# Optimization experiments

Hardware: AMD Instinct MI355X
Metric: run time of the kernel (lower is better)

Reference implementation:

```python
import jax, jax.numpy as jnp
import numpy as np

B, L, E, H, Dff = 2, 2048, 1024, 16, 4096
Dh = E // H


def _ln(x, g, b, eps=1e-5):
    m = jnp.mean(x, axis=-1, keepdims=True)
    v = jnp.mean((x - m) ** 2, axis=-1, keepdims=True)
    return (x - m) / jnp.sqrt(v + eps) * g + b


def setup_inputs() -> dict:
    key = jax.random.key(0)
    ks = jax.random.split(key, 16)
    s_e = 1.0 / np.sqrt(E)
    s_d = 1.0 / np.sqrt(Dff)
    inp = {
        "x": jax.random.normal(ks[0], (B, L, E), jnp.float32),
        # causal mask: positions with 0 are masked out (masked_fill(mask==0, -1e9))
        "mask": jnp.tril(jnp.ones((L, L), jnp.bool_)),
        # per-head QKV projections, stacked over heads: (H, E, Dh), biases (H, Dh)
        "Wq": jax.random.uniform(ks[1], (H, E, Dh), jnp.float32, -s_e, s_e),
        "bq": jax.random.uniform(ks[2], (H, Dh), jnp.float32, -s_e, s_e),
        "Wk": jax.random.uniform(ks[3], (H, E, Dh), jnp.float32, -s_e, s_e),
        "bk": jax.random.uniform(ks[4], (H, Dh), jnp.float32, -s_e, s_e),
        "Wv": jax.random.uniform(ks[5], (H, E, Dh), jnp.float32, -s_e, s_e),
        "bv": jax.random.uniform(ks[6], (H, Dh), jnp.float32, -s_e, s_e),
        "Wo": jax.random.uniform(ks[7], (E, E), jnp.float32, -s_e, s_e),
        "bo": jax.random.uniform(ks[8], (E,), jnp.float32, -s_e, s_e),
        "W1": jax.random.uniform(ks[9], (E, Dff), jnp.float32, -s_e, s_e),
        "c1": jax.random.uniform(ks[10], (Dff,), jnp.float32, -s_e, s_e),
        "W2": jax.random.uniform(ks[11], (Dff, E), jnp.float32, -s_d, s_d),
        "c2": jax.random.uniform(ks[12], (E,), jnp.float32, -s_d, s_d),
        "g1": jnp.ones((E,), jnp.float32),
        "beta1": jnp.zeros((E,), jnp.float32),
        "g2": jnp.ones((E,), jnp.float32),
        "beta2": jnp.zeros((E,), jnp.float32),
    }
    return inp


def reference(x, mask, Wq, bq, Wk, bk, Wv, bv, Wo, bo, W1, c1, W2, c2, g1, beta1, g2, beta2):
    # Batched equivalent of the per-head Attention loop (eval mode: dropout = identity)
    q = jnp.einsum("ble,hed->bhld", x, Wq) + bq[None, :, None, :]
    k = jnp.einsum("ble,hed->bhld", x, Wk) + bk[None, :, None, :]
    v = jnp.einsum("ble,hed->bhld", x, Wv) + bv[None, :, None, :]
    scores = jnp.einsum("bhld,bhmd->bhlm", q, k) / np.sqrt(Dh).astype(np.float32)
    scores = jnp.where(mask[None, None, :, :], scores, -1e9)
    p = jax.nn.softmax(scores, axis=-1)
    z = jnp.einsum("bhlm,bhmd->bhld", p, v)  # (B,H,L,Dh)
    z = z.transpose(0, 2, 1, 3).reshape(B, L, E)  # concat heads
    att = z @ Wo + bo
    h = _ln(x + att, g1, beta1)
    ff = jax.nn.relu(h @ W1 + c1) @ W2 + c2
    out = _ln(h + ff, g2, beta2)
    return out
```

## Files before the change

### kernel.cpp

```cpp
#include <hip/hip_runtime.h>
#include <hip/hip_bf16.h>
#include <math.h>

#define B_   2
#define L_   2048
#define E_   1024
#define H_   16
#define DH   64
#define DFF  4096
#define M_   4096
#define APAD 72
#define SCALE_Q 0.18033688011112042f

typedef __attribute__((ext_vector_type(8))) short short8;
typedef __attribute__((ext_vector_type(4))) float f32x4;
typedef __bf16 bf16x8 __attribute__((ext_vector_type(8)));

__device__ __forceinline__ float bf2f(unsigned short u) {
    return __uint_as_float(((unsigned)u) << 16);
}
__device__ __forceinline__ unsigned short f2bf(float f) {
    unsigned u = __float_as_uint(f);
    return (unsigned short)((u + 0x7fff + ((u >> 16) & 1)) >> 16);
}
__device__ __forceinline__ unsigned pk_trunc(float lo, float hi) {
    return (__float_as_uint(lo) >> 16) | (__float_as_uint(hi) & 0xffff0000u);
}

__device__ __forceinline__ void gld16(const unsigned short* g, unsigned short* l) {
    __builtin_amdgcn_global_load_lds(
        (const __attribute__((address_space(1))) void*)g,
        (__attribute__((address_space(3))) void*)l, 16, 0, 0);
}

__global__ __launch_bounds__(256) void prep(const float* __restrict__ x,
                                            const float* __restrict__ Wq,
                                            const float* __restrict__ Wk,
                                            const float* __restrict__ Wv,
                                            const float* __restrict__ bq,
                                            const float* __restrict__ bk,
                                            const float* __restrict__ bv,
                                            const float* __restrict__ Wo,
                                            const float* __restrict__ W1,
                                            const float* __restrict__ W2,
                                            unsigned short* __restrict__ xb,
                                            unsigned short* __restrict__ Wqkvt,
                                            unsigned short* __restrict__ Wot,
                                            unsigned short* __restrict__ W1t,
                                            unsigned short* __restrict__ W2t,
                                            float* __restrict__ bqkv) {
    __shared__ float tile[32][33];
    int bid = blockIdx.x;
    const int t = threadIdx.x;

    if (bid < 4096) {
        int i = (bid * 256 + t) * 4;
        float4 v = *(const float4*)&x[i];
        ushort4 pk = { f2bf(v.x), f2bf(v.y), f2bf(v.z), f2bf(v.w) };
        *(ushort4*)&xb[i] = pk;
        return;
    }
    bid -= 4096;

    const float* in; unsigned short* outp; int R, C, r0, c0; float sc = 1.f;
    if (bid < 3072) {
        int xq = bid & 1, yq = (bid >> 1) & 31, wh = bid >> 6;
        int which = wh >> 4, h = wh & 15;
        in   = (which == 0 ? Wq : which == 1 ? Wk : Wv) + (size_t)h * E_ * DH;
        outp = Wqkvt + ((size_t)which * 1024 + h * 64) * 1024;
        R = E_; C = DH; r0 = yq * 32; c0 = xq * 32;
        if (which == 0) sc = SCALE_Q;
    } else if (bid < 4096) {
        bid -= 3072;
        in = Wo; outp = Wot; R = E_; C = E_;
        c0 = (bid & 31) * 32; r0 = (bid >> 5) * 32;
    } else if (bid < 8192) {
        bid -= 4096;
        in = W1; outp = W1t; R = E_; C = DFF;
        c0 = (bid & 127) * 32; r0 = (bid >> 7) * 32;
    } else if (bid < 12288) {
        bid -= 8192;
        in = W2; outp = W2t; R = DFF; C = E_;
        c0 = (bid & 31) * 32; r0 = (bid >> 5) * 32;
    } else {
        bid -= 12288;
        int n = bid * 256 + t;
        bqkv[n] = n < 1024 ? bq[n] * SCALE_Q : n < 2048 ? bk[n - 1024] : bv[n - 2048];
        return;
    }

    const int tx = t & 31, tq = t >> 5;
#pragma unroll
    for (int s2 = 0; s2 < 4; s2++)
        tile[tq * 4 + s2][tx] = in[(size_t)(r0 + tq * 4 + s2) * C + c0 + tx] * sc;
    __syncthreads();
#pragma unroll
    for (int s2 = 0; s2 < 4; s2++)
        outp[(size_t)(c0 + tq * 4 + s2) * R + r0 + tx] = f2bf(tile[tx][tq * 4 + s2]);
}

__global__ __launch_bounds__(256) void v_transpose_perm(const unsigned short* __restrict__ qkv,
                                                        unsigned short* __restrict__ vtg) {
    __shared__ unsigned short tile[64 * APAD];
    const int t  = threadIdx.x;
    const int kt = blockIdx.x, hh = blockIdx.y, b = blockIdx.z;
    const int rr0 = t >> 3, o8 = (t & 7) * 8, rr1 = rr0 + 32;
    const size_t gbase = ((size_t)b * L_ + kt * 64) * 3072 + 2048 + hh * 64;
    *(short8*)&tile[rr0 * APAD + o8] = *(const short8*)&qkv[gbase + (size_t)rr0 * 3072 + o8];
    *(short8*)&tile[rr1 * APAD + o8] = *(const short8*)&qkv[gbase + (size_t)rr1 * 3072 + o8];
    __syncthreads();
    const size_t obase = ((size_t)(b * H_ + hh) * 64) * (size_t)L_ + kt * 64;
    const int a = t & 15, d0 = (t >> 4) * 4;
#pragma unroll
    for (int s2 = 0; s2 < 4; s2++) {
        int d = d0 + s2;
        ushort4 pk = { tile[(a +  0) * APAD + d], tile[(a + 16) * APAD + d],
                       tile[(a + 32) * APAD + d], tile[(a + 48) * APAD + d] };
        *(ushort4*)&vtg[obase + (size_t)d * L_ + 4 * a] = pk;
    }
}

template <int RELU, int OUT_BF16>
__global__ __launch_bounds__(256) void gemm_bt(const unsigned short* __restrict__ A,
                                               const unsigned short* __restrict__ Bt,
                                               const float* __restrict__ bias,
                                               void* __restrict__ Cout,
                                               int M, int N, int K) {
    __shared__ __align__(16) unsigned short As[2][128 * 32];
    __shared__ __align__(16) unsigned short Bs[2][128 * 32];

    const int t    = threadIdx.x;
    const int lane = t & 63;
    const int w    = t >> 6;
    const int quad = lane >> 4;
    const int l16  = lane & 15;
    const int wm = (w >> 1) * 64, wn = (w & 1) * 64;

    const int lin = blockIdx.x;
    const int xcd = lin & 7, s = lin >> 3;
    const int n0 = (s >> 2) * 128;
    const int m0 = ((xcd << 2) | (s & 3)) * 128;
    const int rowA = t >> 2, offA = (t & 3) * 8, rowA2 = rowA + 64;

    const size_t aoff0 = (size_t)(m0 + rowA)  * K + offA;
    const size_t aoff1 = (size_t)(m0 + rowA2) * K + offA;
    const size_t boff0 = (size_t)(n0 + rowA)  * K + offA;
    const size_t boff1 = (size_t)(n0 + rowA2) * K + offA;

    const int wb0 = w * 512, wb1 = 2048 + w * 512;

    f32x4 acc[4][4];
#pragma unroll
    for (int i = 0; i < 4; i++)
#pragma unroll
        for (int j = 0; j < 4; j++) acc[i][j] = (f32x4){0.f, 0.f, 0.f, 0.f};

    gld16(&A[aoff0],  &As[0][wb0]);
    gld16(&A[aoff1],  &As[0][wb1]);
    gld16(&Bt[boff0], &Bs[0][wb0]);
    gld16(&Bt[boff1], &Bs[0][wb1]);
    __syncthreads();

    int p = 0;
    for (int k0 = 0; k0 < K; k0 += 32, p ^= 1) {
        if (k0 + 32 < K) {
            gld16(&A[aoff0 + k0 + 32],  &As[p ^ 1][wb0]);
            gld16(&A[aoff1 + k0 + 32],  &As[p ^ 1][wb1]);
            gld16(&Bt[boff0 + k0 + 32], &Bs[p ^ 1][wb0]);
            gld16(&Bt[boff1 + k0 + 32], &Bs[p ^ 1][wb1]);
        }

        bf16x8 af[4], bfv[4];
#pragma unroll
        for (int i = 0; i < 4; i++)
            af[i] = *(const bf16x8*)&As[p][(wm + i * 16 + l16) * 32 + quad * 8];
#pragma unroll
        for (int j = 0; j < 4; j++)
            bfv[j] = *(const bf16x8*)&Bs[p][(wn + j * 16 + l16) * 32 + quad * 8];
#pragma unroll
        for (int i = 0; i < 4; i++)
#pragma unroll
            for (int j = 0; j < 4; j++)
                acc[i][j] = __builtin_amdgcn_mfma_f32_16x16x32_bf16(af[i], bfv[j], acc[i][j], 0, 0, 0);

        __syncthreads();
    }

#pragma unroll
    for (int j = 0; j < 4; j++) {
        int col = n0 + wn + j * 16 + l16;
        float bv = bias[col];
#pragma unroll
        for (int i = 0; i < 4; i++) {
            int rowb = m0 + wm + i * 16 + quad * 4;
#pragma unroll
            for (int r = 0; r < 4; r++) {
                float v = acc[i][j][r] + bv;
                if (RELU) v = fmaxf(v, 0.f);
                if (OUT_BF16)
                    ((unsigned short*)Cout)[(size_t)(rowb + r) * N + col] = f2bf(v);
                else
                    ((float*)Cout)[(size_t)(rowb + r) * N + col] = v;
            }
        }
    }
}

__global__ __launch_bounds__(256) void gemm_sk4(const unsigned short* __restrict__ A,
                                                const unsigned short* __restrict__ Bt,
                                                unsigned short* __restrict__ P0,
                                                unsigned short* __restrict__ P1,
                                                unsigned short* __restrict__ P2,
                                                unsigned short* __restrict__ P3,
                                                int M, int N, int K, int Nt) {
    __shared__ __align__(16) unsigned short As[2][128 * 32];
    __shared__ __align__(16) unsigned short Bs[2][128 * 32];

    const int t    = threadIdx.x;
    const int lane = t & 63;
    const int w    = t >> 6;
    const int quad = lane >> 4;
    const int l16  = lane & 15;
    const int wm = (w >> 1) * 64, wn = (w & 1) * 64;

    const int lin = blockIdx.x;
    const int xcd = lin & 7, s = lin >> 3;
    const int mi = s & 3;
    const int r  = s >> 2;
    const int n0 = (r % Nt) * 128;
    const int z  = r / Nt;
    const int m0 = ((xcd << 2) | mi) * 128;

    const int K4 = K >> 2;
    const int kbeg = z * K4;
    unsigned short* C = (z == 0) ? P0 : (z == 1) ? P1 : (z == 2) ? P2 : P3;
    const int rowA = t >> 2, offA = (t & 3) * 8, rowA2 = rowA + 64;

    const size_t aoff0 = (size_t)(m0 + rowA)  * K + offA + kbeg;
    const size_t aoff1 = (size_t)(m0 + rowA2) * K + offA + kbeg;
    const size_t boff0 = (size_t)(n0 + rowA)  * K + offA + kbeg;
    const size_t boff1 = (size_t)(n0 + rowA2) * K + offA + kbeg;

    const int wb0 = w * 512, wb1 = 2048 + w * 512;

    f32x4 acc[4][4];
#pragma unroll
    for (int i = 0; i < 4; i++)
#pragma unroll
        for (int j = 0; j < 4; j++) acc[i][j] = (f32x4){0.f, 0.f, 0.f, 0.f};

    gld16(&A[aoff0],  &As[0][wb0]);
    gld16(&A[aoff1],  &As[0][wb1]);
    gld16(&Bt[boff0], &Bs[0][wb0]);
    gld16(&Bt[boff1], &Bs[0][wb1]);
    __syncthreads();

    int p = 0;
    for (int k0 = 0; k0 < K4; k0 += 32, p ^= 1) {
        if (k0 + 32 < K4) {
            gld16(&A[aoff0 + k0 + 32],  &As[p ^ 1][wb0]);
            gld16(&A[aoff1 + k0 + 32],  &As[p ^ 1][wb1]);
            gld16(&Bt[boff0 + k0 + 32], &Bs[p ^ 1][wb0]);
            gld16(&Bt[boff1 + k0 + 32], &Bs[p ^ 1][wb1]);
        }

        bf16x8 af[4], bfv[4];
#pragma unroll
        for (int i = 0; i < 4; i++)
            af[i] = *(const bf16x8*)&As[p][(wm + i * 16 + l16) * 32 + quad * 8];
#pragma unroll
        for (int j = 0; j < 4; j++)
            bfv[j] = *(const bf16x8*)&Bs[p][(wn + j * 16 + l16) * 32 + quad * 8];
#pragma unroll
        for (int i = 0; i < 4; i++)
#pragma unroll
            for (int j = 0; j < 4; j++)
                acc[i][j] = __builtin_amdgcn_mfma_f32_16x16x32_bf16(af[i], bfv[j], acc[i][j], 0, 0, 0);

        __syncthreads();
    }

#pragma unroll
    for (int j = 0; j < 4; j++) {
        int col = n0 + wn + j * 16 + l16;
#pragma unroll
        for (int i = 0; i < 4; i++) {
            int rowb = m0 + wm + i * 16 + quad * 4;
#pragma unroll
            for (int r2 = 0; r2 < 4; r2++)
                C[(size_t)(rowb + r2) * N + col] = f2bf(acc[i][j][r2]);
        }
    }
}

__global__ __launch_bounds__(256, 3) void attn_mfma(const unsigned short* __restrict__ qkv,
                                                    const unsigned short* __restrict__ vtg,
                                                    unsigned short* __restrict__ zb) {
    __shared__ __align__(16) unsigned short ks[2][64 * APAD];
    __shared__ __align__(16) unsigned short vt[64 * APAD];
    __shared__ __align__(16) unsigned short ps[128 * APAD];

    const int t    = threadIdx.x;
    const int lane = t & 63;
    const int w    = t >> 6;
    const int l16  = lane & 15;
    const int quad = lane >> 4;

    const int lin  = blockIdx.x;
    const int xcd  = lin & 7;
    const int s    = lin >> 3;
    const int hh   = xcd * 2 + (s & 1);
    const int rest = s >> 1;
    const int b    = rest & 1;
    const int qq0  = rest >> 1;
    const int qq   = b ? qq0 : 15 - qq0;

    const size_t rowbase = (size_t)b * L_;
    const size_t vbase   = ((size_t)(b * H_ + hh) * 64) * (size_t)L_;

    bf16x8 qf[2][2];
#pragma unroll
    for (int g = 0; g < 2; g++) {
        size_t qrow = rowbase + qq * 128 + w * 32 + g * 16 + l16;
#pragma unroll
        for (int c = 0; c < 2; c++)
            qf[g][c] = *(const bf16x8*)&qkv[qrow * 3072 + hh * 64 + c * 32 + quad * 8];
    }

    f32x4 o[2][4];
#pragma unroll
    for (int g = 0; g < 2; g++)
#pragma unroll
        for (int j = 0; j < 4; j++) o[g][j] = (f32x4){0.f, 0.f, 0.f, 0.f};
    float l_i[2][4] = {};

    const int rr0 = t >> 3, o8 = (t & 7) * 8, rr1 = rr0 + 32;
    const int ktmax = 2 * qq + 1;

    {
        size_t kg = rowbase * 3072 + 1024 + hh * 64;
        short8 k0 = *(const short8*)&qkv[kg + (size_t)rr0 * 3072 + o8];
        short8 k1 = *(const short8*)&qkv[kg + (size_t)rr1 * 3072 + o8];
        short8 v0 = *(const short8*)&vtg[vbase + (size_t)rr0 * L_ + o8];
        short8 v1 = *(const short8*)&vtg[vbase + (size_t)rr1 * L_ + o8];
        *(short8*)&ks[0][rr0 * APAD + o8] = k0;
        *(short8*)&ks[0][rr1 * APAD + o8] = k1;
        *(short8*)&vt[rr0 * APAD + o8] = v0;
        *(short8*)&vt[rr1 * APAD + o8] = v1;
    }

    short8 kr0, kr1, vr0, vr1;
    for (int kt = 0; kt <= ktmax; kt++) {
        const int p = kt & 1;
        __syncthreads();

        if (kt < ktmax) {
            size_t kg = (rowbase + (kt + 1) * 64) * 3072 + 1024 + hh * 64;
            kr0 = *(const short8*)&qkv[kg + (size_t)rr0 * 3072 + o8];
            kr1 = *(const short8*)&qkv[kg + (size_t)rr1 * 3072 + o8];
            size_t vg = vbase + (kt + 1) * 64;
            vr0 = *(const short8*)&vtg[vg + (size_t)rr0 * L_ + o8];
            vr1 = *(const short8*)&vtg[vg + (size_t)rr1 * L_ + o8];
        }

        f32x4 s4[2][4];
#pragma unroll
        for (int g = 0; g < 2; g++)
#pragma unroll
            for (int j = 0; j < 4; j++) s4[g][j] = (f32x4){0.f, 0.f, 0.f, 0.f};
#pragma unroll
        for (int c = 0; c < 2; c++)
#pragma unroll
            for (int j = 0; j < 4; j++) {
                bf16x8 kf = *(const bf16x8*)&ks[p][(j * 16 + l16) * APAD + c * 32 + quad * 8];
#pragma unroll
                for (int g = 0; g < 2; g++)
                    s4[g][j] = __builtin_amdgcn_mfma_f32_16x16x32_bf16(qf[g][c], kf, s4[g][j], 0, 0, 0);
            }

        if (kt >= 2 * qq) {
#pragma unroll
            for (int g = 0; g < 2; g++)
#pragma unroll
                for (int j = 0; j < 4; j++) {
                    int lk = kt * 64 + j * 16 + l16;
#pragma unroll
                    for (int r = 0; r < 4; r++)
                        if (lk > qq * 128 + w * 32 + g * 16 + quad * 4 + r)
                            s4[g][j][r] = -INFINITY;
                }
        }

#pragma unroll
        for (int g = 0; g < 2; g++)
#pragma unroll
            for (int r = 0; r < 4; r++) {
                float p0 = __builtin_amdgcn_exp2f(s4[g][0][r]);
                float p1 = __builtin_amdgcn_exp2f(s4[g][1][r]);
                float p2 = __builtin_amdgcn_exp2f(s4[g][2][r]);
                float p3 = __builtin_amdgcn_exp2f(s4[g][3][r]);
                l_i[g][r] += (p0 + p1) + (p2 + p3);
                uint2 pk = { pk_trunc(p0, p1), pk_trunc(p2, p3) };
                *(uint2*)&ps[(w * 32 + g * 16 + quad * 4 + r) * APAD + 4 * l16] = pk;
            }

        __builtin_amdgcn_s_waitcnt(0xc07f);

#pragma unroll
        for (int c = 0; c < 2; c++) {
            bf16x8 pf[2];
#pragma unroll
            for (int g = 0; g < 2; g++)
                pf[g] = *(const bf16x8*)&ps[(w * 32 + g * 16 + l16) * APAD + c * 32 + quad * 8];
#pragma unroll
            for (int j = 0; j < 4; j++) {
                bf16x8 vf = *(const bf16x8*)&vt[(j * 16 + l16) * APAD + c * 32 + quad * 8];
#pragma unroll
                for (int g = 0; g < 2; g++)
                    o[g][j] = __builtin_amdgcn_mfma_f32_16x16x32_bf16(pf[g], vf, o[g][j], 0, 0, 0);
            }
        }

        __syncthreads();
        if (kt < ktmax) {
            *(short8*)&ks[p ^ 1][rr0 * APAD + o8] = kr0;
            *(short8*)&ks[p ^ 1][rr1 * APAD + o8] = kr1;
            *(short8*)&vt[rr0 * APAD + o8] = vr0;
            *(short8*)&vt[rr1 * APAD + o8] = vr1;
        }
    }

#pragma unroll
    for (int g = 0; g < 2; g++)
#pragma unroll
        for (int r = 0; r < 4; r++) {
            float l = l_i[g][r];
            l += __shfl_xor(l, 1);
            l += __shfl_xor(l, 2);
            l += __shfl_xor(l, 4);
            l += __shfl_xor(l, 8);
            float inv = 1.f / l;
            size_t row = rowbase + qq * 128 + w * 32 + g * 16 + quad * 4 + r;
#pragma unroll
            for (int j = 0; j < 4; j++)
                zb[row * 1024 + hh * 64 + j * 16 + l16] = f2bf(o[g][j][r] * inv);
        }
}

template <int WRITE_BF16>
__global__ __launch_bounds__(256) void ln5_kernel(const float* __restrict__ a,
                                                  const unsigned short* __restrict__ q0,
                                                  const unsigned short* __restrict__ q1,
                                                  const unsigned short* __restrict__ q2,
                                                  const unsigned short* __restrict__ q3,
                                                  const float* __restrict__ bias,
                                                  const float* __restrict__ g,
                                                  const float* __restrict__ be,
                                                  float* __restrict__ out,
                                                  unsigned short* __restrict__ out_bf) {
    __shared__ float s1[256], s2[256];
    const int row = blockIdx.x;
    const int t   = threadIdx.x;
    const size_t base = (size_t)row * E_ + t * 4;

    float4 ya = *(const float4*)&a[base];
    ushort4 u0 = *(const ushort4*)&q0[base];
    ushort4 u1 = *(const ushort4*)&q1[base];
    ushort4 u2 = *(const ushort4*)&q2[base];
    ushort4 u3 = *(const ushort4*)&q3[base];
    float4 bb = *(const float4*)&bias[t * 4];
    float y0 = ya.x + bb.x + bf2f(u0.x) + bf2f(u1.x) + bf2f(u2.x) + bf2f(u3.x);
    float y1 = ya.y + bb.y + bf2f(u0.y) + bf2f(u1.y) + bf2f(u2.y) + bf2f(u3.y);
    float y2 = ya.z + bb.z + bf2f(u0.z) + bf2f(u1.z) + bf2f(u2.z) + bf2f(u3.z);
    float y3 = ya.w + bb.w + bf2f(u0.w) + bf2f(u1.w) + bf2f(u2.w) + bf2f(u3.w);

    s1[t] = y0 + y1 + y2 + y3;
    s2[t] = y0 * y0 + y1 * y1 + y2 * y2 + y3 * y3;
    __syncthreads();
    for (int off = 128; off > 0; off >>= 1) {
        if (t < off) { s1[t] += s1[t + off]; s2[t] += s2[t + off]; }
        __syncthreads();
    }
    float mean = s1[0] * (1.0f / E_);
    float var  = s2[0] * (1.0f / E_) - mean * mean;
    float rstd = rsqrtf(var + 1e-5f);

    float4 gv = *(const float4*)&g[t * 4];
    float4 bv = *(const float4*)&be[t * 4];
    float4 ov;
    ov.x = (y0 - mean) * rstd * gv.x + bv.x;
    ov.y = (y1 - mean) * rstd * gv.y + bv.y;
    ov.z = (y2 - mean) * rstd * gv.z + bv.z;
    ov.w = (y3 - mean) * rstd * gv.w + bv.w;
    *(float4*)&out[base] = ov;
    if (WRITE_BF16) {
        ushort4 pk = { f2bf(ov.x), f2bf(ov.y), f2bf(ov.z), f2bf(ov.w) };
        *(ushort4*)&out_bf[base] = pk;
    }
}

extern "C" void kernel_launch(void* const* d_in, const int* in_sizes, int n_in,
                              void* d_out, int out_size, void* d_ws, size_t ws_size,
                              hipStream_t stream)
{
    const float* x     = (const float*)d_in[0];
    const float* Wq    = (const float*)d_in[2];
    const float* bq    = (const float*)d_in[3];
    const float* Wk    = (const float*)d_in[4];
    const float* bk    = (const float*)d_in[5];
    const float* Wv    = (const float*)d_in[6];
    const float* bv    = (const float*)d_in[7];
    const float* Wo    = (const float*)d_in[8];
    const float* bo    = (const float*)d_in[9];
    const float* W1    = (const float*)d_in[10];
    const float* c1    = (const float*)d_in[11];
    const float* W2    = (const float*)d_in[12];
    const float* c2    = (const float*)d_in[13];
    const float* g1    = (const float*)d_in[14];
    const float* beta1 = (const float*)d_in[15];
    const float* g2    = (const float*)d_in[16];
    const float* beta2 = (const float*)d_in[17];
    float* out = (float*)d_out;

    const size_t MB = 1024 * 1024;
    char* w = (char*)d_ws;
    unsigned short* xb    = (unsigned short*)(w + 0 * MB);
    unsigned short* Wqkvt = (unsigned short*)(w + 8 * MB);
    unsigned short* Wot   = (unsigned short*)(w + 14 * MB);
    unsigned short* W1t   = (unsigned short*)(w + 16 * MB);
    unsigned short* W2t   = (unsigned short*)(w + 24 * MB);
    float*          bqkv  = (float*)(w + 32 * MB);
    unsigned short* qkv   = (unsigned short*)(w + 33 * MB);
    unsigned short* zb    = (unsigned short*)(w + 57 * MB);
    float*          h     = (float*)(w + 65 * MB);
    unsigned short* vtg   = (unsigned short*)(w + 89 * MB);
    unsigned short* ap0   = (unsigned short*)(w + 33 * MB);
    unsigned short* ap1   = (unsigned short*)(w + 41 * MB);
    unsigned short* ap2   = (unsigned short*)(w + 49 * MB);
    unsigned short* ap3   = (unsigned short*)(w + 89 * MB);
    unsigned short* hb    = (unsigned short*)(w + 0 * MB);
    unsigned short* ff1b  = (unsigned short*)(w + 33 * MB);
    unsigned short* fp0   = (unsigned short*)(w + 0 * MB);
    unsigned short* fp1   = (unsigned short*)(w + 8 * MB);
    unsigned short* fp2   = (unsigned short*)(w + 16 * MB);
    unsigned short* fp3   = (unsigned short*)(w + 81 * MB);

    dim3 blk(256);

    prep<<<dim3(16396), blk, 0, stream>>>(x, Wq, Wk, Wv, bq, bk, bv, Wo, W1, W2,
                                          xb, Wqkvt, Wot, W1t, W2t, bqkv);

    gemm_bt<0, 1><<<dim3(768), blk, 0, stream>>>(xb, Wqkvt, bqkv, qkv, M_, 3072, E_);

    v_transpose_perm<<<dim3(L_ / 64, H_, B_), blk, 0, stream>>>(qkv, vtg);

    attn_mfma<<<dim3(512), blk, 0, stream>>>(qkv, vtg, zb);

    gemm_sk4<<<dim3(1024), blk, 0, stream>>>(zb, Wot, ap0, ap1, ap2, ap3, M_, E_, E_, 8);

    ln5_kernel<1><<<dim3(M_), blk, 0, stream>>>(x, ap0, ap1, ap2, ap3, bo, g1, beta1, h, hb);

    gemm_bt<1, 1><<<dim3(1024), blk, 0, stream>>>(hb, W1t, c1, ff1b, M_, DFF, E_);

    gemm_sk4<<<dim3(1024), blk, 0, stream>>>(ff1b, W2t, fp0, fp1, fp2, fp3, M_, E_, DFF, 8);

    ln5_kernel<0><<<dim3(M_), blk, 0, stream>>>(h, fp0, fp1, fp2, fp3, c2, g2, beta2, out, nullptr);
}
```

Baseline: 377.2 us.

## Replace 128x128 GEMMs with 256x256-tile 8-wave GEMM using swizzled LDS pipeline

Replaces the two 128x128-tile GEMM kernels with one templated 256x256-tile kernel of 512 threads. It uses 128KB of dynamic LDS with a K-step of 64, an XOR-swizzled layout, and a quadrant-wise schedule that overlaps global-to-LDS staging with MFMA. It also adds s_setprio around MFMA blocks and explicit vmcnt/lgkmcnt waits. The aim is to raise data reuse per tile and keep the matrix units busier. The cost is far fewer blocks (192 or 256 on a 256-CU part), so some wave-quantization and occupancy risk.

```diff
diff --git a/kernel.cpp b/kernel.cpp
--- a/kernel.cpp
+++ b/kernel.cpp
@@ -120,177 +120,169 @@
     }
 }
 
-template <int RELU, int OUT_BF16>
-__global__ __launch_bounds__(256) void gemm_bt(const unsigned short* __restrict__ A,
-                                               const unsigned short* __restrict__ Bt,
-                                               const float* __restrict__ bias,
-                                               void* __restrict__ Cout,
-                                               int M, int N, int K) {
-    __shared__ __align__(16) unsigned short As[2][128 * 32];
-    __shared__ __align__(16) unsigned short Bs[2][128 * 32];
+#define BAR() __builtin_amdgcn_s_barrier()
+#define LGKM0() do { asm volatile("s_waitcnt lgkmcnt(0)" ::: "memory"); \
+                     __builtin_amdgcn_sched_barrier(0); } while (0)
+
+#define G256_READ_A(qr) do {                                                  \
+    _Pragma("unroll") for (int mi = 0; mi < 4; mi++)                          \
+    _Pragma("unroll") for (int ks = 0; ks < 2; ks++)                          \
+        afr[mi][ks] = *(const bf16x8*)&As[bb + ((qr) * 128 + aRow + mi * 16) * 64 + (ks ? cs1 : cs0)]; \
+} while (0)
+
+#define G256_READ_B(qc) do {                                                  \
+    _Pragma("unroll") for (int nj = 0; nj < 2; nj++)                          \
+    _Pragma("unroll") for (int ks = 0; ks < 2; ks++)                          \
+        bfr[qc][nj][ks] = *(const bf16x8*)&Bs[bb + ((qc) * 128 + bRow + nj * 16) * 64 + (ks ? cs1 : cs0)]; \
+} while (0)
+
+#define G256_MFMA(qr, qc) do {                                                \
+    __builtin_amdgcn_s_setprio(1);                                            \
+    _Pragma("unroll") for (int mi = 0; mi < 4; mi++)                          \
+    _Pragma("unroll") for (int nj = 0; nj < 2; nj++)                          \
+    _Pragma("unroll") for (int ks = 0; ks < 2; ks++)                          \
+        acc[qr][qc][mi][nj] = __builtin_amdgcn_mfma_f32_16x16x32_bf16(        \
+            afr[mi][ks], bfr[qc][nj][ks], acc[qr][qc][mi][nj], 0, 0, 0);      \
+    __builtin_amdgcn_s_setprio(0);                                            \
+} while (0)
+
+template <int RELU, int SK>
+__global__ __launch_bounds__(512, 2) void gemm256(const unsigned short* __restrict__ A,
+                                                  const unsigned short* __restrict__ Bt,
+                                                  const float* __restrict__ bias,
+                                                  unsigned short* __restrict__ P0,
+                                                  unsigned short* __restrict__ P1,
+                                                  unsigned short* __restrict__ P2,
+                                                  unsigned short* __restrict__ P3,
+                                                  int M, int N, int K) {
+    extern __shared__ __align__(16) unsigned short g_lds[];
+    unsigned short* As = g_lds;
+    unsigned short* Bs = g_lds + 32768;
 
     const int t    = threadIdx.x;
     const int lane = t & 63;
     const int w    = t >> 6;
     const int quad = lane >> 4;
     const int l16  = lane & 15;
-    const int wm = (w >> 1) * 64, wn = (w & 1) * 64;
 
     const int lin = blockIdx.x;
     const int xcd = lin & 7, s = lin >> 3;
-    const int n0 = (s >> 2) * 128;
-    const int m0 = ((xcd << 2) | (s & 3)) * 128;
-    const int rowA = t >> 2, offA = (t & 3) * 8, rowA2 = rowA + 64;
-
-    const size_t aoff0 = (size_t)(m0 + rowA)  * K + offA;
-    const size_t aoff1 = (size_t)(m0 + rowA2) * K + offA;
-    const size_t boff0 = (size_t)(n0 + rowA)  * K + offA;
-    const size_t boff1 = (size_t)(n0 + rowA2) * K + offA;
-
-    const int wb0 = w * 512, wb1 = 2048 + w * 512;
-
-    f32x4 acc[4][4];
-#pragma unroll
-    for (int i = 0; i < 4; i++)
-#pragma unroll
-        for (int j = 0; j < 4; j++) acc[i][j] = (f32x4){0.f, 0.f, 0.f, 0.f};
-
-    gld16(&A[aoff0],  &As[0][wb0]);
-    gld16(&A[aoff1],  &As[0][wb1]);
-    gld16(&Bt[boff0], &Bs[0][wb0]);
-    gld16(&Bt[boff1], &Bs[0][wb1]);
-    __syncthreads();
-
-    int p = 0;
-    for (int k0 = 0; k0 < K; k0 += 32, p ^= 1) {
-        if (k0 + 32 < K) {
-            gld16(&A[aoff0 + k0 + 32],  &As[p ^ 1][wb0]);
-            gld16(&A[aoff1 + k0 + 32],  &As[p ^ 1][wb1]);
-            gld16(&Bt[boff0 + k0 + 32], &Bs[p ^ 1][wb0]);
-            gld16(&Bt[boff1 + k0 + 32], &Bs[p ^ 1][wb1]);
+    const int m0 = ((xcd << 1) | (s & 1)) * 256;
+    const int rest = s >> 1;
+    int n0, kbeg, KT;
+    unsigned short* C;
+    if (SK) {
+        n0 = (rest & 3) * 256;
+        const int z  = rest >> 2;
+        const int K4 = K >> 2;
+        kbeg = z * K4;
+        KT   = K4 >> 6;
+        C = (z == 0) ? P0 : (z == 1) ? P1 : (z == 2) ? P2 : P3;
+    } else {
+        n0 = rest * 256;
+        kbeg = 0;
+        KT   = K >> 6;
+        C = P0;
+    }
+
+    const int srow = t >> 3;
+    const int ksw  = ((t & 7) ^ (srow & 7)) * 8;
+    const size_t aStage = (size_t)(m0 + srow) * K + kbeg + ksw;
+    const size_t bStage = (size_t)(n0 + srow) * K + kbeg + ksw;
+
+    auto stageA = [&](int buf, int h, int v) {
+        size_t g = aStage + (size_t)(h * 128) * K + (size_t)v * 64;
+        unsigned short* l = As + buf * 16384 + h * 8192 + w * 512;
+        gld16(A + g, l);
+        gld16(A + g + (size_t)64 * K, l + 4096);
+    };
+    auto stageB = [&](int buf, int h, int v) {
+        size_t g = bStage + (size_t)(h * 128) * K + (size_t)v * 64;
+        unsigned short* l = Bs + buf * 16384 + h * 8192 + w * 512;
+        gld16(Bt + g, l);
+        gld16(Bt + g + (size_t)64 * K, l + 4096);
+    };
+
+    const int aRow = (w >> 2) * 64 + l16;
+    const int bRow = (w & 3) * 32 + l16;
+    const int cs0  = (quad ^ (l16 & 7)) * 8;
+    const int cs1  = cs0 ^ 32;
+
+    f32x4 acc[2][2][4][2];
+#pragma unroll
+    for (int a1 = 0; a1 < 2; a1++)
+#pragma unroll
+        for (int a2 = 0; a2 < 2; a2++)
+#pragma unroll
+            for (int a3 = 0; a3 < 4; a3++)
+#pragma unroll
+                for (int a4 = 0; a4 < 2; a4++)
+                    acc[a1][a2][a3][a4] = (f32x4){0.f, 0.f, 0.f, 0.f};
+
+    bf16x8 afr[4][2], bfr[2][2][2];
+
+    stageA(0, 0, 0); stageA(0, 1, 0); stageB(0, 0, 0); stageB(0, 1, 0);
+    if (KT > 1) {
+        stageA(1, 0, 1); stageB(1, 0, 1);
+        asm volatile("s_waitcnt vmcnt(4)" ::: "memory");
+    } else {
+        asm volatile("s_waitcnt vmcnt(0)" ::: "memory");
+    }
+    BAR();
+
+    for (int u = 0; u < KT; ++u) {
+        const int bb = (u & 1) * 16384;
+        const int nb = ((u + 1) & 1);
+
+        G256_READ_A(0);
+        G256_READ_B(0);
+        if (u + 1 < KT) stageB(nb, 1, u + 1);
+        BAR(); LGKM0();
+        G256_MFMA(0, 0);
+        BAR();
+
+        G256_READ_B(1);
+        if (u + 1 < KT) stageA(nb, 1, u + 1);
+        BAR(); LGKM0();
+        G256_MFMA(0, 1);
+        BAR();
+
+        G256_READ_A(1);
+        if (u + 2 < KT) stageA(u & 1, 0, u + 2);
+        BAR(); LGKM0();
+        G256_MFMA(1, 0);
+        BAR();
+
+        if (u + 2 < KT) {
+            stageB(u & 1, 0, u + 2);
+            asm volatile("s_waitcnt vmcnt(4)" ::: "memory");
+        } else {
+            asm volatile("s_waitcnt vmcnt(0)" ::: "memory");
         }
-
-        bf16x8 af[4], bfv[4];
-#pragma unroll
-        for (int i = 0; i < 4; i++)
-            af[i] = *(const bf16x8*)&As[p][(wm + i * 16 + l16) * 32 + quad * 8];
-#pragma unroll
-        for (int j = 0; j < 4; j++)
-            bfv[j] = *(const bf16x8*)&Bs[p][(wn + j * 16 + l16) * 32 + quad * 8];
-#pragma unroll
-        for (int i = 0; i < 4; i++)
-#pragma unroll
-            for (int j = 0; j < 4; j++)
-                acc[i][j] = __builtin_amdgcn_mfma_f32_16x16x32_bf16(af[i], bfv[j], acc[i][j], 0, 0, 0);
-
-        __syncthreads();
-    }
-
-#pragma unroll
-    for (int j = 0; j < 4; j++) {
-        int col = n0 + wn + j * 16 + l16;
-        float bv = bias[col];
-#pragma unroll
-        for (int i = 0; i < 4; i++) {
-            int rowb = m0 + wm + i * 16 + quad * 4;
-#pragma unroll
-            for (int r = 0; r < 4; r++) {
-                float v = acc[i][j][r] + bv;
-                if (RELU) v = fmaxf(v, 0.f);
-                if (OUT_BF16)
-                    ((unsigned short*)Cout)[(size_t)(rowb + r) * N + col] = f2bf(v);
-                else
-                    ((float*)Cout)[(size_t)(rowb + r) * N + col] = v;
+        BAR(); LGKM0();
+        G256_MFMA(1, 1);
+        BAR();
+    }
+
+#pragma unroll
+    for (int qr = 0; qr < 2; qr++)
+#pragma unroll
+        for (int qc = 0; qc < 2; qc++)
+#pragma unroll
+            for (int nj = 0; nj < 2; nj++) {
+                const int col = n0 + qc * 128 + (w & 3) * 32 + nj * 16 + l16;
+                const float bv = SK ? 0.f : bias[col];
+#pragma unroll
+                for (int mi = 0; mi < 4; mi++) {
+                    const int row = m0 + qr * 128 + (w >> 2) * 64 + mi * 16 + quad * 4;
+#pragma unroll
+                    for (int r = 0; r < 4; r++) {
+                        float v = acc[qr][qc][mi][nj][r] + bv;
+                        if (RELU) v = fmaxf(v, 0.f);
+                        C[(size_t)(row + r) * N + col] = f2bf(v);
+                    }
+                }
             }
-        }
-    }
-}
-
-__global__ __launch_bounds__(256) void gemm_sk4(const unsigned short* __restrict__ A,
-                                                const unsigned short* __restrict__ Bt,
-                                                unsigned short* __restrict__ P0,
-                                                unsigned short* __restrict__ P1,
-                                                unsigned short* __restrict__ P2,
-                                                unsigned short* __restrict__ P3,
-                                                int M, int N, int K, int Nt) {
-    __shared__ __align__(16) unsigned short As[2][128 * 32];
-    __shared__ __align__(16) unsigned short Bs[2][128 * 32];
-
-    const int t    = threadIdx.x;
-    const int lane = t & 63;
-    const int w    = t >> 6;
-    const int quad = lane >> 4;
-    const int l16  = lane & 15;
-    const int wm = (w >> 1) * 64, wn = (w & 1) * 64;
-
-    const int lin = blockIdx.x;
-    const int xcd = lin & 7, s = lin >> 3;
-    const int mi = s & 3;
-    const int r  = s >> 2;
-    const int n0 = (r % Nt) * 128;
-    const int z  = r / Nt;
-    const int m0 = ((xcd << 2) | mi) * 128;
-
-    const int K4 = K >> 2;
-    const int kbeg = z * K4;
-    unsigned short* C = (z == 0) ? P0 : (z == 1) ? P1 : (z == 2) ? P2 : P3;
-    const int rowA = t >> 2, offA = (t & 3) * 8, rowA2 = rowA + 64;
-
-    const size_t aoff0 = (size_t)(m0 + rowA)  * K + offA + kbeg;
-    const size_t aoff1 = (size_t)(m0 + rowA2) * K + offA + kbeg;
-    const size_t boff0 = (size_t)(n0 + rowA)  * K + offA + kbeg;
-    const size_t boff1 = (size_t)(n0 + rowA2) * K + offA + kbeg;
-
-    const int wb0 = w * 512, wb1 = 2048 + w * 512;
-
-    f32x4 acc[4][4];
-#pragma unroll
-    for (int i = 0; i < 4; i++)
-#pragma unroll
-        for (int j = 0; j < 4; j++) acc[i][j] = (f32x4){0.f, 0.f, 0.f, 0.f};
-
-    gld16(&A[aoff0],  &As[0][wb0]);
-    gld16(&A[aoff1],  &As[0][wb1]);
-    gld16(&Bt[boff0], &Bs[0][wb0]);
-    gld16(&Bt[boff1], &Bs[0][wb1]);
-    __syncthreads();
-
-    int p = 0;
-    for (int k0 = 0; k0 < K4; k0 += 32, p ^= 1) {
-        if (k0 + 32 < K4) {
-            gld16(&A[aoff0 + k0 + 32],  &As[p ^ 1][wb0]);
-            gld16(&A[aoff1 + k0 + 32],  &As[p ^ 1][wb1]);
-            gld16(&Bt[boff0 + k0 + 32], &Bs[p ^ 1][wb0]);
-            gld16(&Bt[boff1 + k0 + 32], &Bs[p ^ 1][wb1]);
-        }
-
-        bf16x8 af[4], bfv[4];
-#pragma unroll
-        for (int i = 0; i < 4; i++)
-            af[i] = *(const bf16x8*)&As[p][(wm + i * 16 + l16) * 32 + quad * 8];
-#pragma unroll
-        for (int j = 0; j < 4; j++)
-            bfv[j] = *(const bf16x8*)&Bs[p][(wn + j * 16 + l16) * 32 + quad * 8];
-#pragma unroll
-        for (int i = 0; i < 4; i++)
-#pragma unroll
-            for (int j = 0; j < 4; j++)
-                acc[i][j] = __builtin_amdgcn_mfma_f32_16x16x32_bf16(af[i], bfv[j], acc[i][j], 0, 0, 0);
-
-        __syncthreads();
-    }
-
-#pragma unroll
-    for (int j = 0; j < 4; j++) {
-        int col = n0 + wn + j * 16 + l16;
-#pragma unroll
-        for (int i = 0; i < 4; i++) {
-            int rowb = m0 + wm + i * 16 + quad * 4;
-#pragma unroll
-            for (int r2 = 0; r2 < 4; r2++)
-                C[(size_t)(rowb + r2) * N + col] = f2bf(acc[i][j][r2]);
-        }
-    }
 }
 
 __global__ __launch_bounds__(256, 3) void attn_mfma(const unsigned short* __restrict__ qkv,
@@ -545,24 +537,44 @@
     unsigned short* fp2   = (unsigned short*)(w + 16 * MB);
     unsigned short* fp3   = (unsigned short*)(w + 81 * MB);
 
+    static bool lds_inited = false;
+    if (!lds_inited) {
+        (void)hipFuncSetAttribute((const void*)&gemm256<0, 0>,
+                                  hipFuncAttributeMaxDynamicSharedMemorySize, 131072);
+        (void)hipFuncSetAttribute((const void*)&gemm256<1, 0>,
+                                  hipFuncAttributeMaxDynamicSharedMemorySize, 131072);
+        (void)hipFuncSetAttribute((const void*)&gemm256<0, 1>,
+                                  hipFuncAttributeMaxDynamicSharedMemorySize, 131072);
+        lds_inited = true;
+    }
+
     dim3 blk(256);
+    dim3 blk2(512);
 
     prep<<<dim3(16396), blk, 0, stream>>>(x, Wq, Wk, Wv, bq, bk, bv, Wo, W1, W2,
                                           xb, Wqkvt, Wot, W1t, W2t, bqkv);
 
-    gemm_bt<0, 1><<<dim3(768), blk, 0, stream>>>(xb, Wqkvt, bqkv, qkv, M_, 3072, E_);
+    gemm256<0, 0><<<dim3(192), blk2, 131072, stream>>>(xb, Wqkvt, bqkv,
+                                                       qkv, nullptr, nullptr, nullptr,
+                                                       M_, 3072, E_);
 
     v_transpose_perm<<<dim3(L_ / 64, H_, B_), blk, 0, stream>>>(qkv, vtg);
 
     attn_mfma<<<dim3(512), blk, 0, stream>>>(qkv, vtg, zb);
 
-    gemm_sk4<<<dim3(1024), blk, 0, stream>>>(zb, Wot, ap0, ap1, ap2, ap3, M_, E_, E_, 8);
+    gemm256<0, 1><<<dim3(256), blk2, 131072, stream>>>(zb, Wot, nullptr,
+                                                       ap0, ap1, ap2, ap3,
+                                                       M_, E_, E_);
 
     ln5_kernel<1><<<dim3(M_), blk, 0, stream>>>(x, ap0, ap1, ap2, ap3, bo, g1, beta1, h, hb);
 
-    gemm_bt<1, 1><<<dim3(1024), blk, 0, stream>>>(hb, W1t, c1, ff1b, M_, DFF, E_);
-
-    gemm_sk4<<<dim3(1024), blk, 0, stream>>>(ff1b, W2t, fp0, fp1, fp2, fp3, M_, E_, DFF, 8);
+    gemm256<1, 0><<<dim3(256), blk2, 131072, stream>>>(hb, W1t, c1,
+                                                       ff1b, nullptr, nullptr, nullptr,
+                                                       M_, DFF, E_);
+
+    gemm256<0, 1><<<dim3(256), blk2, 131072, stream>>>(ff1b, W2t, nullptr,
+                                                       fp0, fp1, fp2, fp3,
+                                                       M_, E_, DFF);
 
     ln5_kernel<0><<<dim3(M_), blk, 0, stream>>>(h, fp0, fp1, fp2, fp3, c2, g2, beta2, out, nullptr);
 }
```

Result: faster. 341.3 us (-9.5%).
